# Kernel optimization log

Measured on AMD Instinct MI355X. Metric: run time of the kernel, lower is better.

The kernel has to match this reference:

```python
import jax, jax.numpy as jnp
import numpy as np

LATENT_DIM = 256
NUM_CODEBOOKS = 8
CODEBOOK_SIZE = 512
SUB_DIM = LATENT_DIM // NUM_CODEBOOKS
COMMIT_W = 0.25
CODEBOOK_W = 1.0


def setup_inputs() -> dict:
    key = jax.random.key(0)
    k1, k2 = jax.random.split(key)
    latents = jax.random.normal(k1, (16, 4096, LATENT_DIM), dtype=jnp.float32)
    patch_mask = jnp.ones((16, 4096), dtype=jnp.float32)
    bound = 1.0 / CODEBOOK_SIZE
    codebooks = jax.random.uniform(
        k2, (NUM_CODEBOOKS, CODEBOOK_SIZE, SUB_DIM),
        minval=-bound, maxval=bound, dtype=jnp.float32)
    return {"latents": latents, "patch_mask": patch_mask, "codebooks": codebooks}


def reference(latents, patch_mask, codebooks):
    B, N, D = latents.shape
    C, K, d = codebooks.shape
    x = latents.reshape(B, N, C, d)  # split per codebook

    # squared L2 distances to every codebook entry: (B, N, C, K)
    dist = ((x ** 2).sum(-1, keepdims=True)
            + (codebooks ** 2).sum(-1)[None, None]
            - 2.0 * jnp.einsum('bncd,ckd->bnck', x, codebooks))
    ids = jnp.argmin(dist, axis=-1)  # (B, N, C) int

    # gather nearest entries: (B, N, C, d)
    quant = codebooks[jnp.arange(C)[None, None, :], ids]

    # mse_loss is a mean over equal-sized tensors per codebook, so the mean of
    # per-codebook means equals one global mean
    commitment_loss = jnp.mean((x - jax.lax.stop_gradient(quant)) ** 2) * COMMIT_W
    codebook_loss = jnp.mean((quant - jax.lax.stop_gradient(x)) ** 2) * CODEBOOK_W

    # perplexity over active (masked) patches, per codebook then averaged
    one_hot = jax.nn.one_hot(ids, K, dtype=latents.dtype)  # (B, N, C, K)
    denom = jnp.maximum(patch_mask.sum(), 1.0)
    avg_probs = jnp.einsum('bnck,bn->ck', one_hot, patch_mask) / denom
    perplexity = jnp.mean(jnp.exp(-(avg_probs * jnp.log(avg_probs + 1e-8)).sum(-1)))

    quant_flat = quant.reshape(B, N, D)
    st_quantized = latents + jax.lax.stop_gradient(quant_flat - latents)
    return ids, quant_flat, st_quantized, commitment_loss, codebook_loss, perplexity
```

## Files before the change

kernel.cpp:

```cpp
#include <hip/hip_runtime.h>
#include <math.h>

#define BB 16
#define NN 4096
#define DD 256
#define CC 8
#define KK 512
#define SD 32
#define NTOK (BB * NN)
#define IDS_N (NTOK * CC)
#define QN (NTOK * DD)
#define OFF_Q   (IDS_N)
#define OFF_ST  (IDS_N + QN)
#define OFF_SC  (IDS_N + 2 * QN)

#define GUARD 6e-5f
#define CAP 65536

#define WS_ZERO (32 + 16384)

typedef float f32x4 __attribute__((ext_vector_type(4)));
typedef short s16x8 __attribute__((ext_vector_type(8)));

__device__ __forceinline__ unsigned short f2bf(float f) {
    unsigned u = __float_as_uint(f);
    u += 0x7fffu + ((u >> 16) & 1u);
    return (unsigned short)(u >> 16);
}
__device__ __forceinline__ float bf2f(unsigned short h) {
    return __uint_as_float(((unsigned)h) << 16);
}
__device__ __forceinline__ void split8(const float4 a, const float4 b,
                                       s16x8& hv, s16x8& lv) {
    unsigned short h;
    h = f2bf(a.x); hv[0]=(short)h; lv[0]=(short)f2bf(a.x - bf2f(h));
    h = f2bf(a.y); hv[1]=(short)h; lv[1]=(short)f2bf(a.y - bf2f(h));
    h = f2bf(a.z); hv[2]=(short)h; lv[2]=(short)f2bf(a.z - bf2f(h));
    h = f2bf(a.w); hv[3]=(short)h; lv[3]=(short)f2bf(a.w - bf2f(h));
    h = f2bf(b.x); hv[4]=(short)h; lv[4]=(short)f2bf(b.x - bf2f(h));
    h = f2bf(b.y); hv[5]=(short)h; lv[5]=(short)f2bf(b.y - bf2f(h));
    h = f2bf(b.z); hv[6]=(short)h; lv[6]=(short)f2bf(b.z - bf2f(h));
    h = f2bf(b.w); hv[7]=(short)h; lv[7]=(short)f2bf(b.w - bf2f(h));
}

__global__ __launch_bounds__(256) void vq_prep(
    const float* __restrict__ cbs, const float* __restrict__ mask,
    float* __restrict__ csqf, double* __restrict__ mask_sum)
{
    __shared__ double red[256];
    const int tid = threadIdx.x;
    const int cell = blockIdx.x * 256 + tid;
    const float* cp = cbs + (size_t)cell * SD;
    double s = 0.0;
    #pragma unroll
    for (int j = 0; j < 8; ++j) {
        float4 v = ((const float4*)cp)[j];
        double a = (double)v.x, b = (double)v.y, c = (double)v.z, d = (double)v.w;
        s = fma(a, a, s); s = fma(b, b, s);
        s = fma(c, c, s); s = fma(d, d, s);
    }
    csqf[cell] = (float)s;

    double m = 0.0;
    for (int i = cell; i < NTOK; i += 4096) m += (double)mask[i];
    red[tid] = m;
    __syncthreads();
    for (int st = 128; st > 0; st >>= 1) {
        if (tid < st) red[tid] += red[tid + st];
        __syncthreads();
    }
    if (tid == 0) atomicAdd(mask_sum, red[0]);
}

__global__ __launch_bounds__(512, 4) void vq_score(
    const float* __restrict__ latents, const float* __restrict__ mask,
    const float* __restrict__ cbs, const float* __restrict__ csq_g,
    float* __restrict__ out, float* __restrict__ hist,
    unsigned* __restrict__ count, unsigned* __restrict__ list)
{
    __shared__ unsigned short s_hi[KK * SD];
    __shared__ unsigned short s_lo[KK * SD];
    __shared__ float  s_csq[KK];
    __shared__ float  s_lhist[KK];
    __shared__ float  s_best[8][32];
    __shared__ float  s_sec[8][32];
    __shared__ int    s_bid[8][32];

    const int tid = threadIdx.x;
    const int c   = blockIdx.x & 7;
    const int tb  = blockIdx.x >> 3;

    {
        const int cw = tid;
        const float* cp = cbs + ((size_t)c * KK + cw) * SD;
        s_csq[cw] = csq_g[c * KK + cw];
        s_lhist[cw] = 0.f;
        const int sw = (cw >> 1) & 3;
        #pragma unroll
        for (int q = 0; q < 4; ++q) {
            float4 a = ((const float4*)cp)[2 * q];
            float4 b = ((const float4*)cp)[2 * q + 1];
            s16x8 hv, lv;
            split8(a, b, hv, lv);
            ((s16x8*)(s_hi + (size_t)cw * SD))[q ^ sw] = hv;
            ((s16x8*)(s_lo + (size_t)cw * SD))[q ^ sw] = lv;
        }
    }
    __syncthreads();

    const int wv   = tid >> 6;
    const int lane = tid & 63;
    const int col  = lane & 15;
    const int kb   = lane >> 4;

    float4 xa[2][2];
    #pragma unroll
    for (int t = 0; t < 2; ++t) {
        const int token = tb * 1024 + wv * 32 + t * 16 + col;
        const float4* xp =
            (const float4*)(latents + (size_t)token * DD + c * SD + kb * 8);
        xa[t][0] = xp[0]; xa[t][1] = xp[1];
    }

    #pragma unroll 1
    for (int p = 0; p < 4; ++p) {
        const int tok0 = tb * 1024 + p * 256 + wv * 32;

        s16x8 ah[2], al[2];
        #pragma unroll
        for (int t = 0; t < 2; ++t) split8(xa[t][0], xa[t][1], ah[t], al[t]);

        if (p < 3) {
            #pragma unroll
            for (int t = 0; t < 2; ++t) {
                const int token = tb * 1024 + (p + 1) * 256 + wv * 32 + t * 16 + col;
                const float4* xp =
                    (const float4*)(latents + (size_t)token * DD + c * SD + kb * 8);
                xa[t][0] = xp[0]; xa[t][1] = xp[1];
            }
        }

        float best[2][4], sec[2][4]; int bid[2][4];
        #pragma unroll
        for (int t = 0; t < 2; ++t)
            #pragma unroll
            for (int r = 0; r < 4; ++r) {
                best[t][r] = 1e30f; sec[t][r] = 1e30f; bid[t][r] = 0;
            }

        for (int nt = 0; nt < 32; ++nt) {
            const int kcol = nt * 16 + col;
            const int slot = kb ^ ((kcol >> 1) & 3);
            const float cs = s_csq[kcol];
            const s16x8 bh = *((const s16x8*)(s_hi + (size_t)kcol * SD + slot * 8));
            const s16x8 bl = *((const s16x8*)(s_lo + (size_t)kcol * SD + slot * 8));
            #pragma unroll
            for (int t = 0; t < 2; ++t) {
                f32x4 acc = {0.f, 0.f, 0.f, 0.f};
                acc = __builtin_amdgcn_mfma_f32_16x16x32_bf16(ah[t], bh, acc, 0, 0, 0);
                acc = __builtin_amdgcn_mfma_f32_16x16x32_bf16(ah[t], bl, acc, 0, 0, 0);
                acc = __builtin_amdgcn_mfma_f32_16x16x32_bf16(al[t], bh, acc, 0, 0, 0);
                #pragma unroll
                for (int r = 0; r < 4; ++r) {
                    const float s = fmaf(-2.f, acc[r], cs);
                    const bool lt = s < best[t][r];
                    bid[t][r]  = lt ? kcol : bid[t][r];
                    sec[t][r]  = __builtin_amdgcn_fmed3f(s, best[t][r], sec[t][r]);
                    best[t][r] = fminf(best[t][r], s);
                }
            }
        }

        #pragma unroll
        for (int m = 1; m <= 8; m <<= 1) {
            #pragma unroll
            for (int t = 0; t < 2; ++t)
                #pragma unroll
                for (int r = 0; r < 4; ++r) {
                    const float ob = __shfl_xor(best[t][r], m, 64);
                    const float os = __shfl_xor(sec[t][r],  m, 64);
                    const int   oi = __shfl_xor(bid[t][r],  m, 64);
                    const float ns = fminf(fmaxf(best[t][r], ob),
                                           fminf(sec[t][r], os));
                    const bool tk = (ob < best[t][r]) ||
                                    (ob == best[t][r] && oi < bid[t][r]);
                    bid[t][r]  = tk ? oi : bid[t][r];
                    best[t][r] = fminf(best[t][r], ob);
                    sec[t][r]  = ns;
                }
        }

        asm volatile("s_waitcnt lgkmcnt(0)" ::: "memory");
        if (col == 0) {
            #pragma unroll
            for (int t = 0; t < 2; ++t)
                #pragma unroll
                for (int r = 0; r < 4; ++r) {
                    const int idx = t * 16 + kb * 4 + r;
                    s_best[wv][idx] = best[t][r];
                    s_sec[wv][idx]  = sec[t][r];
                    s_bid[wv][idx]  = bid[t][r];
                }
        }
        asm volatile("s_waitcnt lgkmcnt(0)" ::: "memory");

        if (lane < 32) {
            const int token = tok0 + lane;
            const float bb  = s_best[wv][lane];
            const float ssv = s_sec[wv][lane];
            const int   bi  = s_bid[wv][lane];
            const bool flag = (ssv - bb) < GUARD;
            out[(size_t)token * CC + c] = (float)bi;
            if (!flag) {
                atomicAdd(&s_lhist[bi], mask[token]);
            } else {
                unsigned slot = atomicAdd(count, 1u);
                if (slot < CAP) list[slot] = ((unsigned)token << 3) | (unsigned)c;
            }
        }
    }

    __syncthreads();
    {
        float v = s_lhist[tid];
        if (v != 0.f) atomicAdd(&hist[c * KK + tid], v);
    }
}

__global__ __launch_bounds__(256) void vq_resolve(
    const float* __restrict__ latents, const float* __restrict__ mask,
    const float* __restrict__ cbs, const float* __restrict__ csq_g,
    float* __restrict__ out, float* __restrict__ hist,
    const unsigned* __restrict__ count, const unsigned* __restrict__ list)
{
    unsigned n = *count; if (n > CAP) n = CAP;
    const int lane = threadIdx.x & 63;
    const int wave = (blockIdx.x << 2) | (threadIdx.x >> 6);
    const int nwav = gridDim.x << 2;
    const int dq = lane & 7;
    const int kk = lane >> 3;

    for (unsigned i = wave; i < n; i += nwav) {
        const unsigned e = list[i];
        const int token = (int)(e >> 3), c = (int)(e & 7u);
        const float* xp = latents + (size_t)token * DD + c * SD;

        const float4 xq = ((const float4*)xp)[dq];
        const double x0 = (double)xq.x, x1 = (double)xq.y;
        const double x2 = (double)xq.z, x3 = (double)xq.w;

        double px = fma(x3, x3, fma(x2, x2, fma(x1, x1, x0 * x0)));
        px += __shfl_xor(px, 1, 64);
        px += __shfl_xor(px, 2, 64);
        px += __shfl_xor(px, 4, 64);
        const float xsqf = (float)px;

        const float* cbase = cbs + (size_t)c * KK * SD;
        const float* csqc  = csq_g + c * KK;

        float best = 1e30f; int bk = kk;
        #pragma unroll 4
        for (int jk = 0; jk < 64; ++jk) {
            const int k = jk * 8 + kk;
            const float4 cv = ((const float4*)(cbase + (size_t)k * SD))[dq];
            double d = fma((double)cv.w, x3, fma((double)cv.z, x2,
                       fma((double)cv.y, x1, (double)cv.x * x0)));
            d += __shfl_xor(d, 1, 64);
            d += __shfl_xor(d, 2, 64);
            d += __shfl_xor(d, 4, 64);
            const float dotf = (float)d;
            const float t1 = xsqf + csqc[k];
            const float dist = t1 - 2.0f * dotf;
            if (dist < best) { best = dist; bk = k; }
        }
        #pragma unroll
        for (int m = 8; m <= 32; m <<= 1) {
            const float od = __shfl_xor(best, m, 64);
            const int   ok = __shfl_xor(bk,   m, 64);
            if (od < best || (od == best && ok < bk)) { best = od; bk = ok; }
        }
        if (lane == 0) {
            out[(size_t)token * CC + c] = (float)bk;
            atomicAdd(&hist[c * KK + bk], mask[token]);
        }
    }
}

__global__ __launch_bounds__(256) void vq_emit(
    const float* __restrict__ latents, const float* __restrict__ cbs,
    float* __restrict__ out, double* __restrict__ mse_sum)
{
    __shared__ double s_red[4];
    const int tid  = threadIdx.x;
    const int lane = tid & 63;
    const int wv   = tid >> 6;
    const int c    = lane >> 3;
    const int dq   = lane & 7;
    const int wave = blockIdx.x * 4 + wv;

    double acc = 0.0;
    for (int token = wave; token < NTOK; token += 8192) {
        const int bi = (int)out[(size_t)token * CC + c];
        const float4 xq = ((const float4*)(latents + (size_t)token * DD))[lane];
        const float4 qv = ((const float4*)(cbs + ((size_t)c * KK + bi) * SD))[dq];
        float4 sv;
        sv.x = xq.x + (qv.x - xq.x);
        sv.y = xq.y + (qv.y - xq.y);
        sv.z = xq.z + (qv.z - xq.z);
        sv.w = xq.w + (qv.w - xq.w);
        ((float4*)(out + OFF_Q  + (size_t)token * DD))[lane] = qv;
        ((float4*)(out + OFF_ST + (size_t)token * DD))[lane] = sv;
        double d;
        d = (double)xq.x - (double)qv.x; acc = fma(d, d, acc);
        d = (double)xq.y - (double)qv.y; acc = fma(d, d, acc);
        d = (double)xq.z - (double)qv.z; acc = fma(d, d, acc);
        d = (double)xq.w - (double)qv.w; acc = fma(d, d, acc);
    }
    #pragma unroll
    for (int off = 32; off > 0; off >>= 1) acc += __shfl_down(acc, off, 64);
    if (lane == 0) s_red[wv] = acc;
    __syncthreads();
    if (tid == 0)
        atomicAdd(mse_sum, s_red[0] + s_red[1] + s_red[2] + s_red[3]);
}

__global__ __launch_bounds__(512) void vq_final(
    const float* __restrict__ hist, const double* __restrict__ mse_sum,
    const double* __restrict__ mask_sum, float* __restrict__ out)
{
    __shared__ double ent[CC];
    const int tid = threadIdx.x;
    double denom = *mask_sum; if (denom < 1.0) denom = 1.0;

    const int w = tid >> 6;
    const int lane = tid & 63;
    double t = 0.0;
    for (int k = lane; k < KK; k += 64) {
        double p = (double)hist[w * KK + k] / denom;
        t += p * log(p + 1e-8);
    }
    #pragma unroll
    for (int off = 32; off > 0; off >>= 1) t += __shfl_down(t, off, 64);
    if (lane == 0) ent[w] = -t;
    __syncthreads();

    if (tid == 0) {
        double mean = mse_sum[0] / (double)QN;
        out[OFF_SC + 0] = (float)(0.25 * mean);
        out[OFF_SC + 1] = (float)(1.0 * mean);
        double perp = 0.0;
        for (int cc = 0; cc < CC; ++cc) perp += exp(ent[cc]);
        out[OFF_SC + 2] = (float)(perp / (double)CC);
    }
}

extern "C" void kernel_launch(void* const* d_in, const int* in_sizes, int n_in,
                              void* d_out, int out_size, void* d_ws, size_t ws_size,
                              hipStream_t stream) {
    const float* latents = (const float*)d_in[0];
    const float* mask    = (const float*)d_in[1];
    const float* cbs     = (const float*)d_in[2];
    float* out = (float*)d_out;

    double*   mse      = (double*)d_ws;
    double*   mask_sum = (double*)((char*)d_ws + 8);
    unsigned* count    = (unsigned*)((char*)d_ws + 16);
    float*    hist     = (float*)((char*)d_ws + 32);
    float*    csqf     = (float*)((char*)d_ws + 32 + 16384);
    unsigned* list     = (unsigned*)((char*)d_ws + 32 + 32768);

    hipMemsetAsync(d_ws, 0, WS_ZERO, stream);

    vq_prep<<<dim3(16), dim3(256), 0, stream>>>(cbs, mask, csqf, mask_sum);
    vq_score<<<dim3(512), dim3(512), 0, stream>>>(
        latents, mask, cbs, csqf, out, hist, count, list);
    vq_resolve<<<dim3(2048), dim3(256), 0, stream>>>(
        latents, mask, cbs, csqf, out, hist, count, list);
    vq_emit<<<dim3(2048), dim3(256), 0, stream>>>(latents, cbs, out, mse);
    vq_final<<<dim3(1), dim3(512), 0, stream>>>(hist, mse, mask_sum, out);
}
```

Baseline: 348.5 us.

## Fuse quantized output emission and codebook norms into the scoring kernel

```diff
diff --git a/kernel.cpp b/kernel.cpp
--- a/kernel.cpp
+++ b/kernel.cpp
@@ -43,40 +43,12 @@
     h = f2bf(b.w); hv[7]=(short)h; lv[7]=(short)f2bf(b.w - bf2f(h));
 }
 
-__global__ __launch_bounds__(256) void vq_prep(
-    const float* __restrict__ cbs, const float* __restrict__ mask,
-    float* __restrict__ csqf, double* __restrict__ mask_sum)
-{
-    __shared__ double red[256];
-    const int tid = threadIdx.x;
-    const int cell = blockIdx.x * 256 + tid;
-    const float* cp = cbs + (size_t)cell * SD;
-    double s = 0.0;
-    #pragma unroll
-    for (int j = 0; j < 8; ++j) {
-        float4 v = ((const float4*)cp)[j];
-        double a = (double)v.x, b = (double)v.y, c = (double)v.z, d = (double)v.w;
-        s = fma(a, a, s); s = fma(b, b, s);
-        s = fma(c, c, s); s = fma(d, d, s);
-    }
-    csqf[cell] = (float)s;
-
-    double m = 0.0;
-    for (int i = cell; i < NTOK; i += 4096) m += (double)mask[i];
-    red[tid] = m;
-    __syncthreads();
-    for (int st = 128; st > 0; st >>= 1) {
-        if (tid < st) red[tid] += red[tid + st];
-        __syncthreads();
-    }
-    if (tid == 0) atomicAdd(mask_sum, red[0]);
-}
-
 __global__ __launch_bounds__(512, 4) void vq_score(
     const float* __restrict__ latents, const float* __restrict__ mask,
-    const float* __restrict__ cbs, const float* __restrict__ csq_g,
-    float* __restrict__ out, float* __restrict__ hist,
-    unsigned* __restrict__ count, unsigned* __restrict__ list)
+    const float* __restrict__ cbs, float* __restrict__ csq_g,
+    float* __restrict__ out, double* __restrict__ mse_sum,
+    float* __restrict__ hist, unsigned* __restrict__ count,
+    unsigned* __restrict__ list)
 {
     __shared__ unsigned short s_hi[KK * SD];
     __shared__ unsigned short s_lo[KK * SD];
@@ -85,6 +57,7 @@
     __shared__ float  s_best[8][32];
     __shared__ float  s_sec[8][32];
     __shared__ int    s_bid[8][32];
+    __shared__ double s_mse[8];
 
     const int tid = threadIdx.x;
     const int c   = blockIdx.x & 7;
@@ -93,18 +66,29 @@
     {
         const int cw = tid;
         const float* cp = cbs + ((size_t)c * KK + cw) * SD;
-        s_csq[cw] = csq_g[c * KK + cw];
         s_lhist[cw] = 0.f;
         const int sw = (cw >> 1) & 3;
+        double sacc = 0.0;
         #pragma unroll
         for (int q = 0; q < 4; ++q) {
             float4 a = ((const float4*)cp)[2 * q];
             float4 b = ((const float4*)cp)[2 * q + 1];
+            sacc = fma((double)a.x, (double)a.x, sacc);
+            sacc = fma((double)a.y, (double)a.y, sacc);
+            sacc = fma((double)a.z, (double)a.z, sacc);
+            sacc = fma((double)a.w, (double)a.w, sacc);
+            sacc = fma((double)b.x, (double)b.x, sacc);
+            sacc = fma((double)b.y, (double)b.y, sacc);
+            sacc = fma((double)b.z, (double)b.z, sacc);
+            sacc = fma((double)b.w, (double)b.w, sacc);
             s16x8 hv, lv;
             split8(a, b, hv, lv);
             ((s16x8*)(s_hi + (size_t)cw * SD))[q ^ sw] = hv;
             ((s16x8*)(s_lo + (size_t)cw * SD))[q ^ sw] = lv;
         }
+        const float cs = (float)sacc;
+        s_csq[cw] = cs;
+        if (tb == 0) csq_g[c * KK + cw] = cs;
     }
     __syncthreads();
 
@@ -121,6 +105,8 @@
             (const float4*)(latents + (size_t)token * DD + c * SD + kb * 8);
         xa[t][0] = xp[0]; xa[t][1] = xp[1];
     }
+
+    double mseTot = 0.0;
 
     #pragma unroll 1
     for (int p = 0; p < 4; ++p) {
@@ -204,23 +190,62 @@
         }
         asm volatile("s_waitcnt lgkmcnt(0)" ::: "memory");
 
-        if (lane < 32) {
-            const int token = tok0 + lane;
-            const float bb  = s_best[wv][lane];
-            const float ssv = s_sec[wv][lane];
-            const int   bi  = s_bid[wv][lane];
+        {
+            const int tl    = lane >> 1;
+            const int half  = lane & 1;
+            const int token = tok0 + tl;
+            const float bb  = s_best[wv][tl];
+            const float ssv = s_sec[wv][tl];
+            const int   bi  = s_bid[wv][tl];
             const bool flag = (ssv - bb) < GUARD;
-            out[(size_t)token * CC + c] = (float)bi;
-            if (!flag) {
-                atomicAdd(&s_lhist[bi], mask[token]);
-            } else {
-                unsigned slot = atomicAdd(count, 1u);
-                if (slot < CAP) list[slot] = ((unsigned)token << 3) | (unsigned)c;
-            }
-        }
-    }
-
+
+            const float* qp = cbs + ((size_t)c * KK + bi) * SD + half * 16;
+            const float* xp = latents + (size_t)token * DD + c * SD + half * 16;
+            float* oq  = out + OFF_Q  + (size_t)token * DD + c * SD + half * 16;
+            float* ost = out + OFF_ST + (size_t)token * DD + c * SD + half * 16;
+            double acc = 0.0;
+            #pragma unroll
+            for (int j = 0; j < 4; ++j) {
+                float4 qv = ((const float4*)qp)[j];
+                float4 xv = ((const float4*)xp)[j];
+                f32x4 qe, se;
+                qe[0] = qv.x; qe[1] = qv.y; qe[2] = qv.z; qe[3] = qv.w;
+                se[0] = xv.x + (qv.x - xv.x);
+                se[1] = xv.y + (qv.y - xv.y);
+                se[2] = xv.z + (qv.z - xv.z);
+                se[3] = xv.w + (qv.w - xv.w);
+                double d;
+                d = (double)xv.x - (double)qv.x; acc = fma(d, d, acc);
+                d = (double)xv.y - (double)qv.y; acc = fma(d, d, acc);
+                d = (double)xv.z - (double)qv.z; acc = fma(d, d, acc);
+                d = (double)xv.w - (double)qv.w; acc = fma(d, d, acc);
+                __builtin_nontemporal_store(qe, (f32x4*)oq + j);
+                __builtin_nontemporal_store(se, (f32x4*)ost + j);
+            }
+            if (!flag) mseTot += acc;
+            if (half == 0) {
+                out[(size_t)token * CC + c] = (float)bi;
+                if (!flag) {
+                    atomicAdd(&s_lhist[bi], mask[token]);
+                } else {
+                    unsigned slot = atomicAdd(count, 1u);
+                    if (slot < CAP) list[slot] = ((unsigned)token << 3) | (unsigned)c;
+                }
+            }
+        }
+    }
+
+    #pragma unroll
+    for (int off = 32; off > 0; off >>= 1)
+        mseTot += __shfl_down(mseTot, off, 64);
+    if (lane == 0) s_mse[wv] = mseTot;
     __syncthreads();
+    if (tid == 0) {
+        double s = 0.0;
+        #pragma unroll
+        for (int w = 0; w < 8; ++w) s += s_mse[w];
+        atomicAdd(mse_sum, s);
+    }
     {
         float v = s_lhist[tid];
         if (v != 0.f) atomicAdd(&hist[c * KK + tid], v);
@@ -230,8 +255,9 @@
 __global__ __launch_bounds__(256) void vq_resolve(
     const float* __restrict__ latents, const float* __restrict__ mask,
     const float* __restrict__ cbs, const float* __restrict__ csq_g,
-    float* __restrict__ out, float* __restrict__ hist,
-    const unsigned* __restrict__ count, const unsigned* __restrict__ list)
+    float* __restrict__ out, double* __restrict__ mse_sum,
+    float* __restrict__ hist, const unsigned* __restrict__ count,
+    const unsigned* __restrict__ list)
 {
     unsigned n = *count; if (n > CAP) n = CAP;
     const int lane = threadIdx.x & 63;
@@ -279,61 +305,67 @@
             const int   ok = __shfl_xor(bk,   m, 64);
             if (od < best || (od == best && ok < bk)) { best = od; bk = ok; }
         }
+
+        const float4 q4 = ((const float4*)(cbase + (size_t)bk * SD))[dq];
+
+        const int oldid = (int)out[(size_t)token * CC + c];
+        if (bk != oldid) {
+            if (lane == 0) out[(size_t)token * CC + c] = (float)bk;
+            if (kk == 0) {
+                float4 sv;
+                sv.x = xq.x + (q4.x - xq.x);
+                sv.y = xq.y + (q4.y - xq.y);
+                sv.z = xq.z + (q4.z - xq.z);
+                sv.w = xq.w + (q4.w - xq.w);
+                ((float4*)(out + OFF_Q  + (size_t)token * DD + c * SD))[dq] = q4;
+                ((float4*)(out + OFF_ST + (size_t)token * DD + c * SD))[dq] = sv;
+            }
+        }
+        double dd = 0.0;
+        if (kk == 0) {
+            double d;
+            d = (double)xq.x - (double)q4.x; dd = fma(d, d, dd);
+            d = (double)xq.y - (double)q4.y; dd = fma(d, d, dd);
+            d = (double)xq.z - (double)q4.z; dd = fma(d, d, dd);
+            d = (double)xq.w - (double)q4.w; dd = fma(d, d, dd);
+        }
+        dd += __shfl_xor(dd, 1, 64);
+        dd += __shfl_xor(dd, 2, 64);
+        dd += __shfl_xor(dd, 4, 64);
         if (lane == 0) {
-            out[(size_t)token * CC + c] = (float)bk;
+            atomicAdd(mse_sum, dd);
             atomicAdd(&hist[c * KK + bk], mask[token]);
         }
     }
-}
-
-__global__ __launch_bounds__(256) void vq_emit(
-    const float* __restrict__ latents, const float* __restrict__ cbs,
-    float* __restrict__ out, double* __restrict__ mse_sum)
-{
-    __shared__ double s_red[4];
-    const int tid  = threadIdx.x;
-    const int lane = tid & 63;
-    const int wv   = tid >> 6;
-    const int c    = lane >> 3;
-    const int dq   = lane & 7;
-    const int wave = blockIdx.x * 4 + wv;
-
-    double acc = 0.0;
-    for (int token = wave; token < NTOK; token += 8192) {
-        const int bi = (int)out[(size_t)token * CC + c];
-        const float4 xq = ((const float4*)(latents + (size_t)token * DD))[lane];
-        const float4 qv = ((const float4*)(cbs + ((size_t)c * KK + bi) * SD))[dq];
-        float4 sv;
-        sv.x = xq.x + (qv.x - xq.x);
-        sv.y = xq.y + (qv.y - xq.y);
-        sv.z = xq.z + (qv.z - xq.z);
-        sv.w = xq.w + (qv.w - xq.w);
-        ((float4*)(out + OFF_Q  + (size_t)token * DD))[lane] = qv;
-        ((float4*)(out + OFF_ST + (size_t)token * DD))[lane] = sv;
-        double d;
-        d = (double)xq.x - (double)qv.x; acc = fma(d, d, acc);
-        d = (double)xq.y - (double)qv.y; acc = fma(d, d, acc);
-        d = (double)xq.z - (double)qv.z; acc = fma(d, d, acc);
-        d = (double)xq.w - (double)qv.w; acc = fma(d, d, acc);
-    }
-    #pragma unroll
-    for (int off = 32; off > 0; off >>= 1) acc += __shfl_down(acc, off, 64);
-    if (lane == 0) s_red[wv] = acc;
-    __syncthreads();
-    if (tid == 0)
-        atomicAdd(mse_sum, s_red[0] + s_red[1] + s_red[2] + s_red[3]);
 }
 
 __global__ __launch_bounds__(512) void vq_final(
     const float* __restrict__ hist, const double* __restrict__ mse_sum,
-    const double* __restrict__ mask_sum, float* __restrict__ out)
+    const float* __restrict__ mask, float* __restrict__ out)
 {
     __shared__ double ent[CC];
+    __shared__ double s_m[8];
+    __shared__ double s_denom;
     const int tid = threadIdx.x;
-    double denom = *mask_sum; if (denom < 1.0) denom = 1.0;
-
     const int w = tid >> 6;
     const int lane = tid & 63;
+
+    double m = 0.0;
+    for (int i = tid; i < NTOK; i += 512) m += (double)mask[i];
+    #pragma unroll
+    for (int off = 32; off > 0; off >>= 1) m += __shfl_down(m, off, 64);
+    if (lane == 0) s_m[w] = m;
+    __syncthreads();
+    if (tid == 0) {
+        double d = 0.0;
+        #pragma unroll
+        for (int i = 0; i < 8; ++i) d += s_m[i];
+        if (d < 1.0) d = 1.0;
+        s_denom = d;
+    }
+    __syncthreads();
+    const double denom = s_denom;
+
     double t = 0.0;
     for (int k = lane; k < KK; k += 64) {
         double p = (double)hist[w * KK + k] / denom;
@@ -362,20 +394,17 @@
     const float* cbs     = (const float*)d_in[2];
     float* out = (float*)d_out;
 
-    double*   mse      = (double*)d_ws;
-    double*   mask_sum = (double*)((char*)d_ws + 8);
-    unsigned* count    = (unsigned*)((char*)d_ws + 16);
-    float*    hist     = (float*)((char*)d_ws + 32);
-    float*    csqf     = (float*)((char*)d_ws + 32 + 16384);
-    unsigned* list     = (unsigned*)((char*)d_ws + 32 + 32768);
+    double*   mse   = (double*)d_ws;
+    unsigned* count = (unsigned*)((char*)d_ws + 16);
+    float*    hist  = (float*)((char*)d_ws + 32);
+    float*    csqf  = (float*)((char*)d_ws + 32 + 16384);
+    unsigned* list  = (unsigned*)((char*)d_ws + 32 + 32768);
 
     hipMemsetAsync(d_ws, 0, WS_ZERO, stream);
 
-    vq_prep<<<dim3(16), dim3(256), 0, stream>>>(cbs, mask, csqf, mask_sum);
     vq_score<<<dim3(512), dim3(512), 0, stream>>>(
-        latents, mask, cbs, csqf, out, hist, count, list);
+        latents, mask, cbs, csqf, out, mse, hist, count, list);
     vq_resolve<<<dim3(2048), dim3(256), 0, stream>>>(
-        latents, mask, cbs, csqf, out, hist, count, list);
-    vq_emit<<<dim3(2048), dim3(256), 0, stream>>>(latents, cbs, out, mse);
-    vq_final<<<dim3(1), dim3(512), 0, stream>>>(hist, mse, mask_sum, out);
-}
+        latents, mask, cbs, csqf, out, mse, hist, count, list);
+    vq_final<<<dim3(1), dim3(512), 0, stream>>>(hist, mse, mask, out);
+}
```

After: 492.8 us. 41.4% more time.
